# Performance work log

Hardware: AMD Instinct MI355X
Metric: run time of the kernel (lower is better)

The kernel has to match this reference:

```python
import jax, jax.numpy as jnp
import numpy as np

EPS = 1e-5  # BatchNorm2d default eps
HEAD_DIM = 64


def conv1x1_bn_silu(x, w, gamma, beta, mean, var):
    # x: [B, Cin, H, W], w: [Cout, Cin] (1x1 conv, no bias)
    y = jnp.einsum('oc,bchw->bohw', w, x)
    scale = (gamma / jnp.sqrt(var + EPS))[None, :, None, None]
    shift = (beta - mean * gamma / jnp.sqrt(var + EPS))[None, :, None, None]
    y = y * scale + shift
    return y * jax.nn.sigmoid(y)  # SiLU


def setup_inputs() -> dict:
    key = jax.random.key(0)
    ks = jax.random.split(key, 11)
    B, C, H, W = 4, 256, 64, 64
    C3 = 3 * C
    return {
        'x': jax.random.normal(ks[0], (B, C, H, W), jnp.float32),
        'qkv_w': jax.random.normal(ks[1], (C3, C), jnp.float32) * (1.0 / np.sqrt(C)),
        'qkv_gamma': jax.random.uniform(ks[2], (C3,), jnp.float32, 0.5, 1.5),
        'qkv_beta': jax.random.normal(ks[3], (C3,), jnp.float32) * 0.1,
        'qkv_mean': jax.random.normal(ks[4], (C3,), jnp.float32) * 0.1,
        'qkv_var': jax.random.uniform(ks[5], (C3,), jnp.float32, 0.5, 1.5),
        'proj_w': jax.random.normal(ks[6], (C, C), jnp.float32) * (1.0 / np.sqrt(C)),
        'proj_gamma': jax.random.uniform(ks[7], (C,), jnp.float32, 0.5, 1.5),
        'proj_beta': jax.random.normal(ks[8], (C,), jnp.float32) * 0.1,
        'proj_mean': jax.random.normal(ks[9], (C,), jnp.float32) * 0.1,
        'proj_var': jax.random.uniform(ks[10], (C,), jnp.float32, 0.5, 1.5),
    }


def reference(x, qkv_w, qkv_gamma, qkv_beta, qkv_mean, qkv_var,
              proj_w, proj_gamma, proj_beta, proj_mean, proj_var):
    B, C, H, W = x.shape
    hd = HEAD_DIM
    nh = C // hd
    scale = hd ** -0.5

    qkv = conv1x1_bn_silu(x, qkv_w, qkv_gamma, qkv_beta, qkv_mean, qkv_var)
    # [B, 3C, H, W] -> [B, 3, nh, hd, HW] -> (3, B, nh, HW, hd)
    qkv = qkv.reshape(B, 3, nh, hd, H * W).transpose(1, 0, 2, 4, 3)
    q, k, v = qkv[0], qkv[1], qkv[2]  # each [B, nh, HW, hd]

    attn = jnp.einsum('bhqd,bhkd->bhqk', q, k) * scale
    attn = jax.nn.softmax(attn, axis=-1)
    out = jnp.einsum('bhqk,bhkd->bhqd', attn, v)  # [B, nh, HW, hd]
    out = out.transpose(0, 1, 3, 2).reshape(B, C, H, W)

    return conv1x1_bn_silu(out, proj_w, proj_gamma, proj_beta, proj_mean, proj_var)
```

## Files before the change

kernel.cpp:

```cpp
#include <hip/hip_runtime.h>
#include <hip/hip_bf16.h>
#include <math.h>

#define SLEN 4096
#define CIN 256
#define C3 768
#define NH 4
#define HD 64
#define BATCH 4

typedef __attribute__((ext_vector_type(8))) short bf16x8;
typedef __attribute__((ext_vector_type(4))) float f32x4;
typedef __attribute__((ext_vector_type(16))) float f32x16;

__device__ __forceinline__ short f2bf(float f) {
    union { float f; unsigned u; } v; v.f = f;
    unsigned r = v.u + 0x7fff + ((v.u >> 16) & 1);
    return (short)(r >> 16);
}

__device__ __forceinline__ unsigned cvt_pk(float lo, float hi) {
    unsigned r;
    asm("v_cvt_pk_bf16_f32 %0, %1, %2" : "=v"(r) : "v"(lo), "v"(hi));
    return r;
}

__global__ void k_convert_w(const float* __restrict__ qkvw, const float* __restrict__ projw,
                            short* __restrict__ qkvw_bf, short* __restrict__ projw_bf) {
    int i = blockIdx.x * 256 + threadIdx.x;
    if (i < C3 * CIN) qkvw_bf[i] = f2bf(qkvw[i]);
    if (i < CIN * CIN) projw_bf[i] = f2bf(projw[i]);
}

__global__ void k_transpose_x(const float* __restrict__ x, short* __restrict__ xT) {
    __shared__ float t[32][33];
    int b = blockIdx.z;
    int c0 = blockIdx.y * 32, s0 = blockIdx.x * 32;
    int tid = threadIdx.x;
    int r = tid >> 3, c4 = (tid & 7) * 4;
    const float* src = x + ((size_t)b * CIN + c0 + r) * SLEN + s0 + c4;
    float4 v = *reinterpret_cast<const float4*>(src);
    t[r][c4 + 0] = v.x; t[r][c4 + 1] = v.y; t[r][c4 + 2] = v.z; t[r][c4 + 3] = v.w;
    __syncthreads();
    int s_r = tid >> 3, cc = (tid & 7) * 4;
    short4 o = make_short4(f2bf(t[cc + 0][s_r]), f2bf(t[cc + 1][s_r]),
                           f2bf(t[cc + 2][s_r]), f2bf(t[cc + 3][s_r]));
    *reinterpret_cast<short4*>(xT + ((size_t)b * SLEN + s0 + s_r) * CIN + c0 + cc) = o;
}

__launch_bounds__(256)
__global__ void k_qkv(const short* __restrict__ xT, const short* __restrict__ wbf,
                      const float* __restrict__ g, const float* __restrict__ be,
                      const float* __restrict__ mu, const float* __restrict__ va,
                      short* __restrict__ Q, short* __restrict__ Kb, short* __restrict__ Vt) {
    int wv = threadIdx.x >> 6, l = threadIdx.x & 63, lr = l & 15, lg = l >> 4;
    int b = blockIdx.z;
    int s0 = blockIdx.x * 128 + wv * 32;
    int o0 = blockIdx.y * 64;
    f32x4 acc[2][4] = {};
    const short* aptr = xT + ((size_t)b * SLEN + s0 + lr) * CIN + lg * 8;
    const short* bptr = wbf + (size_t)(o0 + lr) * CIN + lg * 8;
#pragma unroll
    for (int k0 = 0; k0 < CIN; k0 += 32) {
        bf16x8 a0 = *(const bf16x8*)(aptr + k0);
        bf16x8 a1 = *(const bf16x8*)(aptr + 16 * CIN + k0);
#pragma unroll
        for (int oj = 0; oj < 4; oj++) {
            bf16x8 bb = *(const bf16x8*)(bptr + oj * 16 * CIN + k0);
            acc[0][oj] = __builtin_amdgcn_mfma_f32_16x16x32_bf16(a0, bb, acc[0][oj], 0, 0, 0);
            acc[1][oj] = __builtin_amdgcn_mfma_f32_16x16x32_bf16(a1, bb, acc[1][oj], 0, 0, 0);
        }
    }
    int which = o0 >> 8;
    int h = (o0 & 255) >> 6;
    int bh = b * NH + h;
    const float QSC = 0.125f * 1.44269504088896f;
#pragma unroll
    for (int oj = 0; oj < 4; oj++) {
        int o = o0 + oj * 16 + lr;
        float sc = g[o] * rsqrtf(va[o] + 1e-5f);
        float sh = be[o] - mu[o] * sc;
        int d = o & 63;
#pragma unroll
        for (int qi = 0; qi < 2; qi++) {
#pragma unroll
            for (int i = 0; i < 4; i++) {
                float y = acc[qi][oj][i] * sc + sh;
                float z = y / (1.f + __expf(-y));
                int s = s0 + qi * 16 + lg * 4 + i;
                if (which == 0) {
                    Q[((size_t)bh * SLEN + s) * HD + d] = f2bf(z * QSC);
                } else if (which == 1) {
                    Kb[((size_t)bh * SLEN + s) * HD + d] = f2bf(z);
                } else {
                    Vt[((size_t)bh * HD + d) * SLEN + s] = f2bf(z);
                }
            }
        }
    }
}

__launch_bounds__(256, 2)
__global__ void k_attn(const short* __restrict__ Q, const short* __restrict__ Kg,
                       const short* __restrict__ Vg, short* __restrict__ aout) {
    __shared__ __align__(16) char lds[16384 + 32768];
    int tid = threadIdx.x;
    int wv = tid >> 6, l = tid & 63;
    int q32 = l & 31;
    int hi  = l >> 5;
    int bh = blockIdx.y;
    int q0 = blockIdx.x * 128 + wv * 32;

    const short* kg = Kg + (size_t)bh * SLEN * HD;
    const short* vg = Vg + (size_t)bh * HD * SLEN;

    bf16x8 qf[4];
    {
        const short* qb = Q + ((size_t)bh * SLEN + q0 + q32) * HD + hi * 8;
        qf[0] = *(const bf16x8*)(qb);
        qf[1] = *(const bf16x8*)(qb + 16);
        qf[2] = *(const bf16x8*)(qb + 32);
        qf[3] = *(const bf16x8*)(qb + 48);
    }

    bf16x8 ones;
#pragma unroll
    for (int e = 0; e < 8; ++e) ones[e] = (short)0x3F80;

    f32x16 oacc0 = {}, oacc1 = {}, sacc = {};
    float mrun = 0.0f, bA = 0.0f, bB = 0.0f;

    int srow = wv * 16 + (l >> 3);
    int gs = l & 7;
    int swz = (l & 7) << 4;
    int soff = srow * 128 + ((gs ^ (l >> 3)) << 4);
    int a0 = q32 * 128 + ((0 * 32 + hi * 16) ^ swz);
    int a1 = q32 * 128 + ((1 * 32 + hi * 16) ^ swz);
    int a2 = q32 * 128 + ((2 * 32 + hi * 16) ^ swz);
    int a3 = q32 * 128 + ((3 * 32 + hi * 16) ^ swz);

    int klane = srow * HD + gs * 8;
    int vlane = srow * SLEN + gs * 8;
    int4 rK0, rK1, rV0, rV1;

#define LOADREG(T) do { \
    const short* kgt = kg + (size_t)(T) * 4096 + klane; \
    rK0 = *(const int4*)(kgt); \
    rK1 = *(const int4*)(kgt + 8 * HD); \
    const short* vgt = vg + (size_t)(T) * 64 + vlane; \
    rV0 = *(const int4*)(vgt); \
    rV1 = *(const int4*)(vgt + 8 * SLEN); \
} while (0)

#define WRITELDS(KB, VB) do { \
    *(int4*)(lds + soff + (KB) * 8192) = rK0; \
    *(int4*)(lds + soff + (KB) * 8192 + 1024) = rK1; \
    *(int4*)(lds + soff + 16384 + (VB) * 8192) = rV0; \
    *(int4*)(lds + soff + 16384 + (VB) * 8192 + 1024) = rV1; \
} while (0)

#define BAR() do { asm volatile("" ::: "memory"); __builtin_amdgcn_s_barrier(); asm volatile("" ::: "memory"); } while (0)
#define WAITBAR() do { asm volatile("s_waitcnt lgkmcnt(0)" ::: "memory"); BAR(); } while (0)

#define MFMA32(A, B, C) __builtin_amdgcn_mfma_f32_32x32x16_bf16(A, B, C)

#define QKT(KB, D0, D1, BSET) do { \
    BSET = mrun; \
    float nb_ = -mrun; \
    _Pragma("unroll") for (int r_ = 0; r_ < 16; ++r_) { D0[r_] = nb_; D1[r_] = nb_; } \
    { \
        bf16x8 k0_, k1_; \
        k0_ = *(const bf16x8*)(lds + a0 + (KB) * 8192); \
        k1_ = *(const bf16x8*)(lds + a0 + (KB) * 8192 + 4096); \
        D0 = __builtin_amdgcn_mfma_f32_32x32x16_bf16(k0_, qf[0], D0, 0, 0, 0); \
        D1 = __builtin_amdgcn_mfma_f32_32x32x16_bf16(k1_, qf[0], D1, 0, 0, 0); \
        k0_ = *(const bf16x8*)(lds + a1 + (KB) * 8192); \
        k1_ = *(const bf16x8*)(lds + a1 + (KB) * 8192 + 4096); \
        D0 = __builtin_amdgcn_mfma_f32_32x32x16_bf16(k0_, qf[1], D0, 0, 0, 0); \
        D1 = __builtin_amdgcn_mfma_f32_32x32x16_bf16(k1_, qf[1], D1, 0, 0, 0); \
        k0_ = *(const bf16x8*)(lds + a2 + (KB) * 8192); \
        k1_ = *(const bf16x8*)(lds + a2 + (KB) * 8192 + 4096); \
        D0 = __builtin_amdgcn_mfma_f32_32x32x16_bf16(k0_, qf[2], D0, 0, 0, 0); \
        D1 = __builtin_amdgcn_mfma_f32_32x32x16_bf16(k1_, qf[2], D1, 0, 0, 0); \
        k0_ = *(const bf16x8*)(lds + a3 + (KB) * 8192); \
        k1_ = *(const bf16x8*)(lds + a3 + (KB) * 8192 + 4096); \
        D0 = __builtin_amdgcn_mfma_f32_32x32x16_bf16(k0_, qf[3], D0, 0, 0, 0); \
        D1 = __builtin_amdgcn_mfma_f32_32x32x16_bf16(k1_, qf[3], D1, 0, 0, 0); \
    } \
} while (0)

#define PVKC(AK, SV, BASE, VB) do { \
    unsigned A0_ = cvt_pk(SV[(BASE) + 0], SV[(BASE) + 1]); \
    unsigned A1_ = cvt_pk(SV[(BASE) + 2], SV[(BASE) + 3]); \
    unsigned A2_ = cvt_pk(SV[(BASE) + 4], SV[(BASE) + 5]); \
    unsigned A3_ = cvt_pk(SV[(BASE) + 6], SV[(BASE) + 7]); \
    asm volatile("v_permlane32_swap_b32 %0, %1" : "+v"(A0_), "+v"(A2_)); \
    asm volatile("v_permlane32_swap_b32 %0, %1" : "+v"(A1_), "+v"(A3_)); \
    union { bf16x8 v; unsigned u[4]; } pf_; \
    pf_.u[0] = A0_; pf_.u[1] = A1_; pf_.u[2] = A2_; pf_.u[3] = A3_; \
    bf16x8 v0_ = *(const bf16x8*)(lds + (AK) + 16384 + (VB) * 8192); \
    bf16x8 v1_ = *(const bf16x8*)(lds + (AK) + 16384 + (VB) * 8192 + 4096); \
    oacc0 = __builtin_amdgcn_mfma_f32_32x32x16_bf16(v0_, pf_.v, oacc0, 0, 0, 0); \
    oacc1 = __builtin_amdgcn_mfma_f32_32x32x16_bf16(v1_, pf_.v, oacc1, 0, 0, 0); \
    sacc  = __builtin_amdgcn_mfma_f32_32x32x16_bf16(ones, pf_.v, sacc, 0, 0, 0); \
} while (0)

#define SMPV(VB, S0, S1, BSET) do { \
    float pa_ = S0[0], pb_ = S0[8], pc_ = S1[0], pd_ = S1[8]; \
    _Pragma("unroll") for (int r_ = 1; r_ < 8; ++r_) { \
        pa_ = fmaxf(pa_, S0[r_]); pb_ = fmaxf(pb_, S0[8 + r_]); \
        pc_ = fmaxf(pc_, S1[r_]); pd_ = fmaxf(pd_, S1[8 + r_]); \
    } \
    float pms_ = fmaxf(fmaxf(pa_, pb_), fmaxf(pc_, pd_)); \
    float c1_ = pms_, c2_ = pms_; \
    asm volatile("" : "+v"(c2_));  \
    asm volatile("v_permlane32_swap_b32 %0, %1" : "+v"(c1_), "+v"(c2_)); \
    pms_ = fmaxf(c1_, c2_); \
    float db_ = mrun - (BSET); \
    if (!__all(pms_ <= db_ + 10.0f)) { \
        float mn_ = fmaxf(mrun, pms_ + (BSET)); \
        float al_ = __builtin_amdgcn_exp2f(mrun - mn_); \
        _Pragma("unroll") for (int r_ = 0; r_ < 16; ++r_) { oacc0[r_] *= al_; oacc1[r_] *= al_; } \
        sacc[0] *= al_; \
        mrun = mn_; db_ = mn_ - (BSET); \
    } \
    if (__all(db_ == 0.0f)) { \
        _Pragma("unroll") for (int r_ = 0; r_ < 16; ++r_) { \
            S0[r_] = __builtin_amdgcn_exp2f(S0[r_]); \
            S1[r_] = __builtin_amdgcn_exp2f(S1[r_]); \
        } \
    } else { \
        _Pragma("unroll") for (int r_ = 0; r_ < 16; ++r_) { \
            S0[r_] = __builtin_amdgcn_exp2f(S0[r_] - db_); \
            S1[r_] = __builtin_amdgcn_exp2f(S1[r_] - db_); \
        } \
    } \
    PVKC(a0, S0, 0, VB); \
    PVKC(a1, S0, 8, VB); \
    PVKC(a2, S1, 0, VB); \
    PVKC(a3, S1, 8, VB); \
} while (0)

    f32x16 sA0, sA1, sB0, sB1;

    LOADREG(0);
    WRITELDS(0, 0);
    LOADREG(1);
    WAITBAR();
    WRITELDS(1, 1);
    LOADREG(2);
    QKT(0, sA0, sA1, bA);
    WAITBAR();

    for (int j = 0; j < 15; ++j) {
        int t = 4 * j + 1;
        WRITELDS(0, 2); LOADREG(t + 2); QKT(1, sB0, sB1, bB); SMPV(0, sA0, sA1, bA); WAITBAR();
        WRITELDS(1, 3); LOADREG(t + 3); QKT(0, sA0, sA1, bA); SMPV(1, sB0, sB1, bB); WAITBAR();
        WRITELDS(0, 0); LOADREG(t + 4); QKT(1, sB0, sB1, bB); SMPV(2, sA0, sA1, bA); WAITBAR();
        WRITELDS(1, 1); LOADREG(t + 5); QKT(0, sA0, sA1, bA); SMPV(3, sB0, sB1, bB); WAITBAR();
    }
    WRITELDS(0, 2); LOADREG(63); QKT(1, sB0, sB1, bB); SMPV(0, sA0, sA1, bA); WAITBAR();
    WRITELDS(1, 3); QKT(0, sA0, sA1, bA); SMPV(1, sB0, sB1, bB); WAITBAR();
    QKT(1, sB0, sB1, bB); SMPV(2, sA0, sA1, bA);
    SMPV(3, sB0, sB1, bB);

    float inv = 1.f / sacc[0];
    int b = bh >> 2, h = bh & 3;
    short* ob = aout + ((size_t)b * SLEN + q0 + q32) * CIN + h * HD;
#pragma unroll
    for (int g4 = 0; g4 < 4; ++g4) {
        uint2 st0, st1;
        st0.x = cvt_pk(oacc0[4 * g4 + 0] * inv, oacc0[4 * g4 + 1] * inv);
        st0.y = cvt_pk(oacc0[4 * g4 + 2] * inv, oacc0[4 * g4 + 3] * inv);
        st1.x = cvt_pk(oacc1[4 * g4 + 0] * inv, oacc1[4 * g4 + 1] * inv);
        st1.y = cvt_pk(oacc1[4 * g4 + 2] * inv, oacc1[4 * g4 + 3] * inv);
        *(uint2*)(ob + 8 * g4 + 4 * hi) = st0;
        *(uint2*)(ob + 32 + 8 * g4 + 4 * hi) = st1;
    }
#undef LOADREG
#undef WRITELDS
#undef BAR
#undef WAITBAR
#undef MFMA32
#undef QKT
#undef PVKC
#undef SMPV
}

__launch_bounds__(256)
__global__ void k_proj(const short* __restrict__ aout, const short* __restrict__ wbf,
                       const float* __restrict__ g, const float* __restrict__ be,
                       const float* __restrict__ mu, const float* __restrict__ va,
                       float* __restrict__ out) {
    int wv = threadIdx.x >> 6, l = threadIdx.x & 63, lr = l & 15, lg = l >> 4;
    int b = blockIdx.z;
    int s0 = blockIdx.x * 128 + wv * 32;
    int o0 = blockIdx.y * 64;
    f32x4 acc[2][4] = {};
    const short* aptr = aout + ((size_t)b * SLEN + s0 + lr) * CIN + lg * 8;
    const short* bptr = wbf + (size_t)(o0 + lr) * CIN + lg * 8;
#pragma unroll
    for (int k0 = 0; k0 < CIN; k0 += 32) {
        bf16x8 a0 = *(const bf16x8*)(aptr + k0);
        bf16x8 a1 = *(const bf16x8*)(aptr + 16 * CIN + k0);
#pragma unroll
        for (int oj = 0; oj < 4; oj++) {
            bf16x8 bb = *(const bf16x8*)(bptr + oj * 16 * CIN + k0);
            acc[0][oj] = __builtin_amdgcn_mfma_f32_16x16x32_bf16(a0, bb, acc[0][oj], 0, 0, 0);
            acc[1][oj] = __builtin_amdgcn_mfma_f32_16x16x32_bf16(a1, bb, acc[1][oj], 0, 0, 0);
        }
    }
#pragma unroll
    for (int oj = 0; oj < 4; oj++) {
        int o = o0 + oj * 16 + lr;
        float sc = g[o] * rsqrtf(va[o] + 1e-5f);
        float sh = be[o] - mu[o] * sc;
#pragma unroll
        for (int qi = 0; qi < 2; qi++) {
            float4 st;
            float* stp = &st.x;
#pragma unroll
            for (int i = 0; i < 4; i++) {
                float y = acc[qi][oj][i] * sc + sh;
                stp[i] = y / (1.f + __expf(-y));
            }
            int s = s0 + qi * 16 + lg * 4;
            *reinterpret_cast<float4*>(out + ((size_t)b * CIN + o) * SLEN + s) = st;
        }
    }
}

extern "C" void kernel_launch(void* const* d_in, const int* in_sizes, int n_in,
                              void* d_out, int out_size, void* d_ws, size_t ws_size,
                              hipStream_t stream) {
    const float* x    = (const float*)d_in[0];
    const float* qkvw = (const float*)d_in[1];
    const float* qg   = (const float*)d_in[2];
    const float* qbe  = (const float*)d_in[3];
    const float* qmu  = (const float*)d_in[4];
    const float* qva  = (const float*)d_in[5];
    const float* pw   = (const float*)d_in[6];
    const float* pg   = (const float*)d_in[7];
    const float* pbe  = (const float*)d_in[8];
    const float* pmu  = (const float*)d_in[9];
    const float* pva  = (const float*)d_in[10];
    float* out = (float*)d_out;

    char* ws = (char*)d_ws;
    short* xT       = (short*)(ws);
    short* qkvw_bf  = (short*)(ws + 8388608);
    short* projw_bf = (short*)(ws + 8781824);
    short* Qb       = (short*)(ws + 8912896);
    short* Kb       = (short*)(ws + 17301504);
    short* Vt       = (short*)(ws + 25690112);
    short* aout     = (short*)(ws + 34078720);

    k_convert_w<<<768, 256, 0, stream>>>(qkvw, pw, qkvw_bf, projw_bf);
    k_transpose_x<<<dim3(128, 8, 4), 256, 0, stream>>>(x, xT);
    k_qkv<<<dim3(32, 12, 4), 256, 0, stream>>>(xT, qkvw_bf, qg, qbe, qmu, qva, Qb, Kb, Vt);
    k_attn<<<dim3(32, 16), 256, 0, stream>>>(Qb, Kb, Vt, aout);
    k_proj<<<dim3(32, 4, 4), 256, 0, stream>>>(aout, projw_bf, pg, pbe, pmu, pva, out);
}
```

Before: 163.5 us.

## Stream K/V tiles directly to LDS, remap blocks per XCD, raise MFMA priority

The attention kernel now copies K and V tiles straight from global memory into LDS with global_load_lds, applying the swizzle on the source address. This replaces the register-staged load-then-store path and its extra VGPRs and ds_write instructions. The 1D grid is remapped so each XCD handles two (batch, head) pairs, which is meant to keep K/V reuse inside one XCD's L2. MFMA sections are also wrapped in s_setprio. The barrier now waits on vmcnt(0) each iteration, so loads are only prefetched one stage ahead and may be less hidden than with the old register double-buffering.

```diff
diff --git a/kernel.cpp b/kernel.cpp
--- a/kernel.cpp
+++ b/kernel.cpp
@@ -12,6 +12,13 @@
 typedef __attribute__((ext_vector_type(8))) short bf16x8;
 typedef __attribute__((ext_vector_type(4))) float f32x4;
 typedef __attribute__((ext_vector_type(16))) float f32x16;
+
+typedef const __attribute__((address_space(1))) void GVoid;
+typedef __attribute__((address_space(3))) void LVoid;
+
+__device__ __forceinline__ void gl2lds16(const void* g, void* l) {
+    __builtin_amdgcn_global_load_lds((GVoid*)g, (LVoid*)l, 16, 0, 0);
+}
 
 __device__ __forceinline__ short f2bf(float f) {
     union { float f; unsigned u; } v; v.f = f;
@@ -108,8 +115,11 @@
     int wv = tid >> 6, l = tid & 63;
     int q32 = l & 31;
     int hi  = l >> 5;
-    int bh = blockIdx.y;
-    int q0 = blockIdx.x * 128 + wv * 32;
+
+    int bid = blockIdx.x;
+    int xcd = bid & 7, slot = bid >> 3;
+    int bh = 2 * xcd + (slot & 1);
+    int q0 = (slot >> 1) * 128 + wv * 32;
 
     const short* kg = Kg + (size_t)bh * SLEN * HD;
     const short* vg = Vg + (size_t)bh * HD * SLEN;
@@ -130,44 +140,37 @@
     f32x16 oacc0 = {}, oacc1 = {}, sacc = {};
     float mrun = 0.0f, bA = 0.0f, bB = 0.0f;
 
-    int srow = wv * 16 + (l >> 3);
-    int gs = l & 7;
+    int colsw = (((l & 7) ^ (l >> 3)) << 4);
+    const char* kgB = (const char*)kg;
+    const char* vgB = (const char*)vg;
+    int ksrc = (wv * 16 + (l >> 3)) * 128 + colsw;
+    int vsrc = (wv * 16 + (l >> 3)) * 8192 + colsw;
+    int wdst = wv * 2048;
+
+#define STAGE(T, KB, VB) do { \
+    gl2lds16(kgB + (size_t)(T) * 8192 + ksrc,          lds + (KB) * 8192 + wdst); \
+    gl2lds16(kgB + (size_t)(T) * 8192 + ksrc + 1024,   lds + (KB) * 8192 + wdst + 1024); \
+    gl2lds16(vgB + (size_t)(T) * 128 + vsrc,           lds + 16384 + (VB) * 8192 + wdst); \
+    gl2lds16(vgB + (size_t)(T) * 128 + vsrc + 65536,   lds + 16384 + (VB) * 8192 + wdst + 1024); \
+} while (0)
+
+#define VMBAR() do { \
+    asm volatile("s_waitcnt vmcnt(0) lgkmcnt(0)" ::: "memory"); \
+    __builtin_amdgcn_s_barrier(); \
+    asm volatile("" ::: "memory"); \
+} while (0)
+
     int swz = (l & 7) << 4;
-    int soff = srow * 128 + ((gs ^ (l >> 3)) << 4);
     int a0 = q32 * 128 + ((0 * 32 + hi * 16) ^ swz);
     int a1 = q32 * 128 + ((1 * 32 + hi * 16) ^ swz);
     int a2 = q32 * 128 + ((2 * 32 + hi * 16) ^ swz);
     int a3 = q32 * 128 + ((3 * 32 + hi * 16) ^ swz);
 
-    int klane = srow * HD + gs * 8;
-    int vlane = srow * SLEN + gs * 8;
-    int4 rK0, rK1, rV0, rV1;
-
-#define LOADREG(T) do { \
-    const short* kgt = kg + (size_t)(T) * 4096 + klane; \
-    rK0 = *(const int4*)(kgt); \
-    rK1 = *(const int4*)(kgt + 8 * HD); \
-    const short* vgt = vg + (size_t)(T) * 64 + vlane; \
-    rV0 = *(const int4*)(vgt); \
-    rV1 = *(const int4*)(vgt + 8 * SLEN); \
-} while (0)
-
-#define WRITELDS(KB, VB) do { \
-    *(int4*)(lds + soff + (KB) * 8192) = rK0; \
-    *(int4*)(lds + soff + (KB) * 8192 + 1024) = rK1; \
-    *(int4*)(lds + soff + 16384 + (VB) * 8192) = rV0; \
-    *(int4*)(lds + soff + 16384 + (VB) * 8192 + 1024) = rV1; \
-} while (0)
-
-#define BAR() do { asm volatile("" ::: "memory"); __builtin_amdgcn_s_barrier(); asm volatile("" ::: "memory"); } while (0)
-#define WAITBAR() do { asm volatile("s_waitcnt lgkmcnt(0)" ::: "memory"); BAR(); } while (0)
-
-#define MFMA32(A, B, C) __builtin_amdgcn_mfma_f32_32x32x16_bf16(A, B, C)
-
 #define QKT(KB, D0, D1, BSET) do { \
     BSET = mrun; \
     float nb_ = -mrun; \
     _Pragma("unroll") for (int r_ = 0; r_ < 16; ++r_) { D0[r_] = nb_; D1[r_] = nb_; } \
+    __builtin_amdgcn_s_setprio(1); \
     { \
         bf16x8 k0_, k1_; \
         k0_ = *(const bf16x8*)(lds + a0 + (KB) * 8192); \
@@ -187,6 +190,7 @@
         D0 = __builtin_amdgcn_mfma_f32_32x32x16_bf16(k0_, qf[3], D0, 0, 0, 0); \
         D1 = __builtin_amdgcn_mfma_f32_32x32x16_bf16(k1_, qf[3], D1, 0, 0, 0); \
     } \
+    __builtin_amdgcn_s_setprio(0); \
 } while (0)
 
 #define PVKC(AK, SV, BASE, VB) do { \
@@ -235,32 +239,30 @@
             S1[r_] = __builtin_amdgcn_exp2f(S1[r_] - db_); \
         } \
     } \
+    __builtin_amdgcn_s_setprio(1); \
     PVKC(a0, S0, 0, VB); \
     PVKC(a1, S0, 8, VB); \
     PVKC(a2, S1, 0, VB); \
     PVKC(a3, S1, 8, VB); \
+    __builtin_amdgcn_s_setprio(0); \
 } while (0)
 
     f32x16 sA0, sA1, sB0, sB1;
 
-    LOADREG(0);
-    WRITELDS(0, 0);
-    LOADREG(1);
-    WAITBAR();
-    WRITELDS(1, 1);
-    LOADREG(2);
+    STAGE(0, 0, 0);
+    VMBAR();
+    STAGE(1, 1, 1);
     QKT(0, sA0, sA1, bA);
-    WAITBAR();
+    VMBAR();
 
     for (int j = 0; j < 15; ++j) {
-        int t = 4 * j + 1;
-        WRITELDS(0, 2); LOADREG(t + 2); QKT(1, sB0, sB1, bB); SMPV(0, sA0, sA1, bA); WAITBAR();
-        WRITELDS(1, 3); LOADREG(t + 3); QKT(0, sA0, sA1, bA); SMPV(1, sB0, sB1, bB); WAITBAR();
-        WRITELDS(0, 0); LOADREG(t + 4); QKT(1, sB0, sB1, bB); SMPV(2, sA0, sA1, bA); WAITBAR();
-        WRITELDS(1, 1); LOADREG(t + 5); QKT(0, sA0, sA1, bA); SMPV(3, sB0, sB1, bB); WAITBAR();
-    }
-    WRITELDS(0, 2); LOADREG(63); QKT(1, sB0, sB1, bB); SMPV(0, sA0, sA1, bA); WAITBAR();
-    WRITELDS(1, 3); QKT(0, sA0, sA1, bA); SMPV(1, sB0, sB1, bB); WAITBAR();
+        STAGE(4 * j + 2, 0, 2); QKT(1, sB0, sB1, bB); SMPV(0, sA0, sA1, bA); VMBAR();
+        STAGE(4 * j + 3, 1, 3); QKT(0, sA0, sA1, bA); SMPV(1, sB0, sB1, bB); VMBAR();
+        STAGE(4 * j + 4, 0, 0); QKT(1, sB0, sB1, bB); SMPV(2, sA0, sA1, bA); VMBAR();
+        STAGE(4 * j + 5, 1, 1); QKT(0, sA0, sA1, bA); SMPV(3, sB0, sB1, bB); VMBAR();
+    }
+    STAGE(62, 0, 2); QKT(1, sB0, sB1, bB); SMPV(0, sA0, sA1, bA); VMBAR();
+    STAGE(63, 1, 3); QKT(0, sA0, sA1, bA); SMPV(1, sB0, sB1, bB); VMBAR();
     QKT(1, sB0, sB1, bB); SMPV(2, sA0, sA1, bA);
     SMPV(3, sB0, sB1, bB);
 
@@ -277,11 +279,8 @@
         *(uint2*)(ob + 8 * g4 + 4 * hi) = st0;
         *(uint2*)(ob + 32 + 8 * g4 + 4 * hi) = st1;
     }
-#undef LOADREG
-#undef WRITELDS
-#undef BAR
-#undef WAITBAR
-#undef MFMA32
+#undef STAGE
+#undef VMBAR
 #undef QKT
 #undef PVKC
 #undef SMPV
@@ -358,6 +357,6 @@
     k_convert_w<<<768, 256, 0, stream>>>(qkvw, pw, qkvw_bf, projw_bf);
     k_transpose_x<<<dim3(128, 8, 4), 256, 0, stream>>>(x, xT);
     k_qkv<<<dim3(32, 12, 4), 256, 0, stream>>>(xT, qkvw_bf, qg, qbe, qmu, qva, Qb, Kb, Vt);
-    k_attn<<<dim3(32, 16), 256, 0, stream>>>(Qb, Kb, Vt, aout);
+    k_attn<<<512, 256, 0, stream>>>(Qb, Kb, Vt, aout);
     k_proj<<<dim3(32, 4, 4), 256, 0, stream>>>(aout, projw_bf, pg, pbe, pmu, pva, out);
 }
```

After: 159.7 us. 1.02x faster.
